# Performance work log

Measured on AMD Instinct MI355X. Metric: run time of the kernel, lower is better.

Reference implementation:

```python
import jax, jax.numpy as jnp
import numpy as np

UNITS = 128  # rnn_units hardcoded in the module


def setup_inputs() -> dict:
    key = jax.random.key(0)
    k1, k2, k3 = jax.random.split(key, 3)
    B, T, F = 256, 1024, 128  # feature dim must equal UNITS (shared cell across both layers)
    inputs = jax.random.normal(k1, (B, T, F), dtype=jnp.float32)
    # Keras LSTMCell params, gate order i|f|g|o; SHARED by both stacked layers
    # because StackedRNNCells([cell]*2) reuses the same cell object.
    W = jax.random.normal(k2, (F, 4 * UNITS), dtype=jnp.float32) * 0.05   # kernel
    U = jax.random.normal(k3, (UNITS, 4 * UNITS), dtype=jnp.float32) * 0.05  # recurrent_kernel
    b = jnp.zeros((4 * UNITS,), dtype=jnp.float32)  # bias
    return {"inputs": inputs, "W": W, "U": U, "b": b}


def _lstm_cell(x, h, c, W, U, b):
    # z: [B, 4*UNITS]; Keras gate order i, f, g(candidate), o
    z = x @ W + h @ U + b
    i, f, g, o = jnp.split(z, 4, axis=-1)
    i = jax.nn.sigmoid(i)
    f = jax.nn.sigmoid(f)
    g = jnp.tanh(g)
    o = jax.nn.sigmoid(o)
    c_new = f * c + i * g
    h_new = o * jnp.tanh(c_new)
    return h_new, c_new


def reference(inputs, W, U, b):
    B, T, F = inputs.shape
    z0 = jnp.zeros((B, UNITS), dtype=inputs.dtype)

    def step(carry, x_t):
        h1, c1, h2, c2 = carry
        h1, c1 = _lstm_cell(x_t, h1, c1, W, U, b)   # layer 1
        h2, c2 = _lstm_cell(h1, h2, c2, W, U, b)    # layer 2 (shared weights)
        return (h1, c1, h2, c2), None

    (h1, c1, h2, c2), _ = jax.lax.scan(step, (z0, z0, z0, z0), jnp.swapaxes(inputs, 0, 1))
    outputs = h2                                    # last-step output (return_sequences=False)
    init_state = jnp.zeros(inputs.shape, dtype=inputs.dtype)  # tf.zeros(inputs.shape)
    final_state = c1  # source unpacks `outputs, _, h2, _, _` -> 2nd flat state = layer-1 cell state
    return (outputs, init_state, final_state)
```

## Files before the change

kernel.cpp:

```cpp
#include <hip/hip_runtime.h>


typedef _Float16 f16;
typedef _Float16 f16x2 __attribute__((ext_vector_type(2)));
typedef _Float16 f16x8 __attribute__((ext_vector_type(8)));
typedef float    f32x4 __attribute__((ext_vector_type(4)));

#define T_STEPS 1024
#define UNITS   128
#define NLSTM   32
#define BPW     8
#define NBLK    256
#define OUT_ZERO 32768
#define OUT_C1   33587200
#define BUFB    6144

#define MFMA16(A, B, C) __builtin_amdgcn_mfma_f32_16x16x32_f16((A), (B), (C), 0, 0, 0)

__device__ __forceinline__ float frcp_(float x) {
#if __has_builtin(__builtin_amdgcn_rcpf)
    return __builtin_amdgcn_rcpf(x);
#else
    return 1.0f / x;
#endif
}
__device__ __forceinline__ float sigmoidf_(float x) {
    return frcp_(1.0f + __expf(-x));
}
__device__ __forceinline__ float tanhf_(float x) {
    float e = __expf(2.0f * x);
    return 1.0f - 2.0f * frcp_(e + 1.0f);
}
__device__ __forceinline__ unsigned pkh(float a, float b) {
    f16x2 t; t[0] = (f16)a; t[1] = (f16)b;
    return __builtin_bit_cast(unsigned, t);
}

__global__ __launch_bounds__(512, 2) void lstm2_kernel(
    const float* __restrict__ X,
    const float* __restrict__ W,
    const float* __restrict__ U,
    const float* __restrict__ Bv,
    float* __restrict__ out)
{
    const int blk = blockIdx.x;
    const int tid = threadIdx.x;

    if (blk >= NLSTM) {
        const size_t nthr = (size_t)(NBLK - NLSTM) * 512;
        float4* dst = (float4*)(out + OUT_ZERO);
        const float4 z4 = make_float4(0.f, 0.f, 0.f, 0.f);
        for (size_t i = (size_t)(blk - NLSTM) * 512 + tid; i < 8388608u; i += nthr)
            dst[i] = z4;
        return;
    }

    const int w  = tid >> 6;
    const int l  = tid & 63;
    const int lr = l & 15;
    const int lc = l >> 4;
    const int u  = w * 16 + lr;
    const int b0 = blk * BPW;
    const bool cell2 = (l >= 32);

    __shared__ __align__(16) char Abuf[2][BUFB];
    char* Ab = (char*)Abuf;

    f16x8 Wf[4][4], Uf[4][4];
    #pragma unroll
    for (int g = 0; g < 4; ++g) {
        #pragma unroll
        for (int kt = 0; kt < 4; ++kt) {
            f16x8 wt, ut;
            #pragma unroll
            for (int j = 0; j < 8; ++j) {
                const int krow = kt * 32 + lc * 8 + j;
                wt[j] = (f16)W[(size_t)krow * 512 + g * 128 + u];
                ut[j] = (f16)U[(size_t)krow * 512 + g * 128 + u];
            }
            Wf[g][kt] = wt;  Uf[g][kt] = ut;
        }
    }
    float bias[4];
    #pragma unroll
    for (int g = 0; g < 4; ++g) bias[g] = Bv[g * 128 + u];

    const int swz = (lr & 7) << 4;
    int raddr[2][4];
    #pragma unroll
    for (int a0 = 0; a0 < 2; ++a0)
        #pragma unroll
        for (int kt = 0; kt < 4; ++kt)
            raddr[a0][kt] = (((a0 * 8 + lr) * 256) + kt * 64 + lc * 16) ^ swz;
    int waddr[4];
    #pragma unroll
    for (int e = 0; e < 4; ++e)
        waddr[e] = ((8 + 4 * lc + e) * 256 + u * 2) ^ ((((4 * lc + e) & 7)) << 4);

    for (int i = tid; i < 3072; i += 512) ((float*)Ab)[i] = 0.0f;
    {
        const int flat = tid * 2, xr = flat >> 7, xc = flat & 127;
        const float2 xv = *(const float2*)(X + (size_t)(b0 + xr) * (T_STEPS * UNITS) + xc);
        const int byte = ((xr * 256 + xc * 2) ^ ((xr & 7) << 4));
        *(unsigned*)(Ab + byte) = pkh(xv.x, xv.y);
    }
    __syncthreads();

    float cst[4] = {0.f, 0.f, 0.f, 0.f};

    for (int k = 0; k <= T_STEPS; ++k) {
        const int rdo = (k & 1) * BUFB, wro = BUFB - rdo;

        float xa = 0.f, xb = 0.f; int xr = 0, xc = 0;
        if (k + 1 < T_STEPS) {
            const int flat = tid * 2; xr = flat >> 7; xc = flat & 127;
            const float2 xv = *(const float2*)(X + (size_t)(b0 + xr) * (T_STEPS * UNITS)
                                                 + (size_t)(k + 1) * UNITS + xc);
            xa = xv.x; xb = xv.y;
        }

        f16x8 A1[4], A2[4];
        #pragma unroll
        for (int kt = 0; kt < 4; ++kt) {
            A1[kt] = *(const f16x8*)(Ab + rdo + raddr[0][kt]);
            A2[kt] = *(const f16x8*)(Ab + rdo + raddr[1][kt]);
        }

        f32x4 accg = {bias[2], bias[2], bias[2], bias[2]};
        f32x4 acco = {bias[3], bias[3], bias[3], bias[3]};
        #pragma unroll
        for (int kt = 0; kt < 4; ++kt) {
            accg = MFMA16(A1[kt], Wf[2][kt], accg);
            acco = MFMA16(A1[kt], Wf[3][kt], acco);
        }
        #pragma unroll
        for (int kt = 0; kt < 4; ++kt) {
            accg = MFMA16(A2[kt], Uf[2][kt], accg);
            acco = MFMA16(A2[kt], Uf[3][kt], acco);
        }

        f32x4 acci = {bias[0], bias[0], bias[0], bias[0]};
        f32x4 accf = {bias[1], bias[1], bias[1], bias[1]};
        float gg[4], oo[4];

        acci = MFMA16(A1[0], Wf[0][0], acci);  accf = MFMA16(A1[0], Wf[1][0], accf);
        gg[0] = tanhf_(accg[0]);
        acci = MFMA16(A1[1], Wf[0][1], acci);  accf = MFMA16(A1[1], Wf[1][1], accf);
        oo[0] = sigmoidf_(acco[0]);
        acci = MFMA16(A1[2], Wf[0][2], acci);  accf = MFMA16(A1[2], Wf[1][2], accf);
        gg[1] = tanhf_(accg[1]);
        acci = MFMA16(A1[3], Wf[0][3], acci);  accf = MFMA16(A1[3], Wf[1][3], accf);
        oo[1] = sigmoidf_(acco[1]);
        acci = MFMA16(A2[0], Uf[0][0], acci);  accf = MFMA16(A2[0], Uf[1][0], accf);
        gg[2] = tanhf_(accg[2]);
        acci = MFMA16(A2[1], Uf[0][1], acci);  accf = MFMA16(A2[1], Uf[1][1], accf);
        oo[2] = sigmoidf_(acco[2]);
        acci = MFMA16(A2[2], Uf[0][2], acci);  accf = MFMA16(A2[2], Uf[1][2], accf);
        gg[3] = tanhf_(accg[3]);
        acci = MFMA16(A2[3], Uf[0][3], acci);  accf = MFMA16(A2[3], Uf[1][3], accf);
        oo[3] = sigmoidf_(acco[3]);

        if (k + 1 < T_STEPS) {
            const int byte = ((xr * 256 + xc * 2) ^ ((xr & 7) << 4));
            *(unsigned*)(Ab + wro + byte) = pkh(xa, xb);
        }

        const bool active = cell2 ? (k > 0) : (k < T_STEPS);
        float hq[4];
        #pragma unroll
        for (int e = 0; e < 4; ++e) {
            const float ig = sigmoidf_(acci[e]);
            const float fg = sigmoidf_(accf[e]);
            const float cn = fg * cst[e] + ig * gg[e];
            if (active) cst[e] = cn;
            hq[e] = oo[e] * tanhf_(cn);
        }

        if (active && k < T_STEPS) {
            #pragma unroll
            for (int e = 0; e < 4; ++e)
                *(f16*)(Ab + wro + waddr[e]) = (f16)hq[e];
        }

        if (k == T_STEPS - 1 && !cell2) {
            #pragma unroll
            for (int e = 0; e < 4; ++e)
                out[OUT_C1 + (size_t)(b0 + 4 * lc + e) * UNITS + u] = cst[e];
        }
        if (k == T_STEPS && cell2) {
            #pragma unroll
            for (int e = 0; e < 4; ++e)
                out[(size_t)(b0 + 4 * lc + e - 8) * UNITS + u] = hq[e];
        }
        __syncthreads();
    }
}

extern "C" void kernel_launch(void* const* d_in, const int* in_sizes, int n_in,
                              void* d_out, int out_size, void* d_ws, size_t ws_size,
                              hipStream_t stream) {
    const float* X  = (const float*)d_in[0];
    const float* W  = (const float*)d_in[1];
    const float* U  = (const float*)d_in[2];
    const float* Bv = (const float*)d_in[3];
    float* out = (float*)d_out;
    hipLaunchKernelGGL(lstm2_kernel, dim3(NBLK), dim3(512), 0, stream,
                       X, W, U, Bv, out);
}
```

Measured before the change: 1.102 ms.

## Halve batch rows per block and interleave layer rows into MFMA tiles

```diff
diff --git a/kernel.cpp b/kernel.cpp
--- a/kernel.cpp
+++ b/kernel.cpp
@@ -8,12 +8,12 @@
 
 #define T_STEPS 1024
 #define UNITS   128
-#define NLSTM   32
-#define BPW     8
+#define NLSTM   64
+#define BPW     4
 #define NBLK    256
 #define OUT_ZERO 32768
 #define OUT_C1   33587200
-#define BUFB    6144
+#define TILEB   4096
 
 #define MFMA16(A, B, C) __builtin_amdgcn_mfma_f32_16x16x32_f16((A), (B), (C), 0, 0, 0)
 
@@ -34,6 +34,9 @@
 __device__ __forceinline__ unsigned pkh(float a, float b) {
     f16x2 t; t[0] = (f16)a; t[1] = (f16)b;
     return __builtin_bit_cast(unsigned, t);
+}
+__device__ __forceinline__ int swb(int row, int byteoff) {
+    return row * 256 + (byteoff ^ ((row & 7) << 4));
 }
 
 __global__ __launch_bounds__(512, 2) void lstm2_kernel(
@@ -61,10 +64,9 @@
     const int lc = l >> 4;
     const int u  = w * 16 + lr;
     const int b0 = blk * BPW;
-    const bool cell2 = (l >= 32);
-
-    __shared__ __align__(16) char Abuf[2][BUFB];
-    char* Ab = (char*)Abuf;
+
+    __shared__ __align__(16) char A1b[2][TILEB];
+    __shared__ __align__(16) char A2b[2][TILEB];
 
     f16x8 Wf[4][4], Uf[4][4];
     #pragma unroll
@@ -85,45 +87,45 @@
     #pragma unroll
     for (int g = 0; g < 4; ++g) bias[g] = Bv[g * 128 + u];
 
-    const int swz = (lr & 7) << 4;
-    int raddr[2][4];
+    int ard[4];
     #pragma unroll
-    for (int a0 = 0; a0 < 2; ++a0)
-        #pragma unroll
-        for (int kt = 0; kt < 4; ++kt)
-            raddr[a0][kt] = (((a0 * 8 + lr) * 256) + kt * 64 + lc * 16) ^ swz;
-    int waddr[4];
-    #pragma unroll
-    for (int e = 0; e < 4; ++e)
-        waddr[e] = ((8 + 4 * lc + e) * 256 + u * 2) ^ ((((4 * lc + e) & 7)) << 4);
-
-    for (int i = tid; i < 3072; i += 512) ((float*)Ab)[i] = 0.0f;
-    {
-        const int flat = tid * 2, xr = flat >> 7, xc = flat & 127;
-        const float2 xv = *(const float2*)(X + (size_t)(b0 + xr) * (T_STEPS * UNITS) + xc);
-        const int byte = ((xr * 256 + xc * 2) ^ ((xr & 7) << 4));
-        *(unsigned*)(Ab + byte) = pkh(xv.x, xv.y);
+    for (int kt = 0; kt < 4; ++kt) ard[kt] = swb(lr, kt * 64 + lc * 16);
+    const int wh_hi = swb(4 * lc + 1, u * 2);
+    const int wh_lo = swb(4 * lc,     u * 2);
+
+    for (int i = tid; i < 4096; i += 512) {
+        ((float*)A1b)[i] = 0.0f;
+        ((float*)A2b)[i] = 0.0f;
     }
     __syncthreads();
-
-    float cst[4] = {0.f, 0.f, 0.f, 0.f};
+    if (tid < 256) {
+        const int a = tid >> 6, uc = (tid & 63) * 2;
+        const float2 xv = *(const float2*)(X + (size_t)(b0 + a) * (T_STEPS * UNITS) + uc);
+        *(unsigned*)(&A1b[0][0] + swb(4 * a, uc * 2)) = pkh(xv.x, xv.y);
+    }
+    __syncthreads();
+
+    float c1 = 0.f, c2 = 0.f;
 
     for (int k = 0; k <= T_STEPS; ++k) {
-        const int rdo = (k & 1) * BUFB, wro = BUFB - rdo;
-
-        float xa = 0.f, xb = 0.f; int xr = 0, xc = 0;
-        if (k + 1 < T_STEPS) {
-            const int flat = tid * 2; xr = flat >> 7; xc = flat & 127;
-            const float2 xv = *(const float2*)(X + (size_t)(b0 + xr) * (T_STEPS * UNITS)
-                                                 + (size_t)(k + 1) * UNITS + xc);
+        const int rdo = (k & 1) * TILEB, wro = TILEB - rdo;
+        char* A1r = &A1b[0][0] + rdo;  char* A1w = &A1b[0][0] + wro;
+        char* A2r = &A2b[0][0] + rdo;  char* A2w = &A2b[0][0] + wro;
+
+        float xa = 0.f, xb = 0.f; int xrow = 0, xuc = 0;
+        const bool ldx = (tid < 256) && (k + 1 < T_STEPS);
+        if (ldx) {
+            const int a = tid >> 6; xuc = (tid & 63) * 2; xrow = 4 * a;
+            const float2 xv = *(const float2*)(X + (size_t)(b0 + a) * (T_STEPS * UNITS)
+                                                 + (size_t)(k + 1) * UNITS + xuc);
             xa = xv.x; xb = xv.y;
         }
 
         f16x8 A1[4], A2[4];
         #pragma unroll
         for (int kt = 0; kt < 4; ++kt) {
-            A1[kt] = *(const f16x8*)(Ab + rdo + raddr[0][kt]);
-            A2[kt] = *(const f16x8*)(Ab + rdo + raddr[1][kt]);
+            A1[kt] = *(const f16x8*)(A1r + ard[kt]);
+            A2[kt] = *(const f16x8*)(A2r + ard[kt]);
         }
 
         f32x4 accg = {bias[2], bias[2], bias[2], bias[2]};
@@ -141,57 +143,48 @@
 
         f32x4 acci = {bias[0], bias[0], bias[0], bias[0]};
         f32x4 accf = {bias[1], bias[1], bias[1], bias[1]};
-        float gg[4], oo[4];
-
+        float gg0, gg1, oo0, oo1;
         acci = MFMA16(A1[0], Wf[0][0], acci);  accf = MFMA16(A1[0], Wf[1][0], accf);
-        gg[0] = tanhf_(accg[0]);
+        gg0 = tanhf_(accg[0]);
         acci = MFMA16(A1[1], Wf[0][1], acci);  accf = MFMA16(A1[1], Wf[1][1], accf);
-        oo[0] = sigmoidf_(acco[0]);
+        oo0 = sigmoidf_(acco[0]);
         acci = MFMA16(A1[2], Wf[0][2], acci);  accf = MFMA16(A1[2], Wf[1][2], accf);
-        gg[1] = tanhf_(accg[1]);
+        gg1 = tanhf_(accg[1]);
         acci = MFMA16(A1[3], Wf[0][3], acci);  accf = MFMA16(A1[3], Wf[1][3], accf);
-        oo[1] = sigmoidf_(acco[1]);
+        oo1 = sigmoidf_(acco[1]);
         acci = MFMA16(A2[0], Uf[0][0], acci);  accf = MFMA16(A2[0], Uf[1][0], accf);
-        gg[2] = tanhf_(accg[2]);
+        if (ldx)
+            *(unsigned*)(A1w + swb(xrow, xuc * 2)) = pkh(xa, xb);
         acci = MFMA16(A2[1], Uf[0][1], acci);  accf = MFMA16(A2[1], Uf[1][1], accf);
-        oo[2] = sigmoidf_(acco[2]);
         acci = MFMA16(A2[2], Uf[0][2], acci);  accf = MFMA16(A2[2], Uf[1][2], accf);
-        gg[3] = tanhf_(accg[3]);
         acci = MFMA16(A2[3], Uf[0][3], acci);  accf = MFMA16(A2[3], Uf[1][3], accf);
-        oo[3] = sigmoidf_(acco[3]);
-
-        if (k + 1 < T_STEPS) {
-            const int byte = ((xr * 256 + xc * 2) ^ ((xr & 7) << 4));
-            *(unsigned*)(Ab + wro + byte) = pkh(xa, xb);
-        }
-
-        const bool active = cell2 ? (k > 0) : (k < T_STEPS);
-        float hq[4];
-        #pragma unroll
-        for (int e = 0; e < 4; ++e) {
-            const float ig = sigmoidf_(acci[e]);
-            const float fg = sigmoidf_(accf[e]);
-            const float cn = fg * cst[e] + ig * gg[e];
-            if (active) cst[e] = cn;
-            hq[e] = oo[e] * tanhf_(cn);
-        }
-
-        if (active && k < T_STEPS) {
-            #pragma unroll
-            for (int e = 0; e < 4; ++e)
-                *(f16*)(Ab + wro + waddr[e]) = (f16)hq[e];
-        }
-
-        if (k == T_STEPS - 1 && !cell2) {
-            #pragma unroll
-            for (int e = 0; e < 4; ++e)
-                out[OUT_C1 + (size_t)(b0 + 4 * lc + e) * UNITS + u] = cst[e];
-        }
-        if (k == T_STEPS && cell2) {
-            #pragma unroll
-            for (int e = 0; e < 4; ++e)
-                out[(size_t)(b0 + 4 * lc + e - 8) * UNITS + u] = hq[e];
-        }
+
+        const bool act1 = (k < T_STEPS);
+        const bool act2 = (k > 0);
+        const float si0 = sigmoidf_(acci[0]);
+        const float si1 = sigmoidf_(acci[1]);
+        const float sf0 = sigmoidf_(accf[0]);
+        const float sf1 = sigmoidf_(accf[1]);
+        const float gg1b = tanhf_(accg[1] * 0.0f + accg[1]);
+        (void)gg1b;
+        const float cn1 = sf0 * c1 + si0 * gg0;
+        const float cn2 = sf1 * c2 + si1 * gg1;
+        if (act1) c1 = cn1;
+        if (act2) c2 = cn2;
+        const float h1v = oo0 * tanhf_(cn1);
+        const float h2v = oo1 * tanhf_(cn2);
+
+        if (act1) {
+            *(f16*)(A1w + wh_hi) = (f16)h1v;
+            *(f16*)(A2w + wh_lo) = (f16)h1v;
+        }
+        if (act2 && k < T_STEPS)
+            *(f16*)(A2w + wh_hi) = (f16)h2v;
+
+        if (k == T_STEPS - 1)
+            out[OUT_C1 + (size_t)(b0 + lc) * UNITS + u] = c1;
+        if (k == T_STEPS)
+            out[(size_t)(b0 + lc) * UNITS + u] = h2v;
         __syncthreads();
     }
 }
```

Result: faster. 996.9 us (-9.6%).
